# Kernel optimization log

Measured on AMD Instinct MI355X. Metric: run time of the kernel, lower is better.

Reference implementation:

```python
import jax, jax.numpy as jnp
import numpy as np

N_NODES = 100000
IMPROVED_FILL = 2.0  # PyG improved=True self-loop weight


def setup_inputs() -> dict:
    key = jax.random.key(0)
    k1, k2, k3, k4 = jax.random.split(key, 4)
    x = jax.random.normal(k1, (N_NODES, 128), dtype=jnp.float32)
    edge_index = jax.random.randint(k2, (2, 1600000), 0, N_NODES, dtype=jnp.int64)
    edge_weight = jax.random.uniform(k3, (1600000,), dtype=jnp.float32)
    W = jax.random.normal(k4, (128, 64), dtype=jnp.float32) * (1.0 / np.sqrt(128.0))
    b = jnp.zeros((64,), dtype=jnp.float32)
    return {"x": x, "edge_index": edge_index, "edge_weight": edge_weight, "W": W, "b": b}


def reference(x, edge_index, edge_weight, W, b):
    N = x.shape[0]
    row, col = edge_index[0], edge_index[1]
    # add self-loops with fill value 2.0 (improved=True)
    loop = jnp.arange(N, dtype=edge_index.dtype)
    row_f = jnp.concatenate([row, loop])
    col_f = jnp.concatenate([col, loop])
    ew_f = jnp.concatenate([edge_weight, jnp.full((N,), IMPROVED_FILL, dtype=x.dtype)])
    # symmetric degree normalization (degree computed at target/col, per PyG gcn_norm)
    deg = jax.ops.segment_sum(ew_f, col_f, num_segments=N)  # [N]
    dinv = jnp.where(deg > 0, jax.lax.rsqrt(deg), 0.0)
    norm = dinv[row_f] * ew_f * dinv[col_f]  # [E+N]
    # linear transform first, then gather-scale-scatter aggregation, then bias
    xw = x @ W  # [N, 64]
    msgs = xw[row_f] * norm[:, None]  # [E+N, 64]
    out = jax.ops.segment_sum(msgs, col_f, num_segments=N) + b  # [N, 64]
    # act is None -> returns (x, embedding), both equal to out
    return (out, out)
```

## Files before the change

kernel.cpp:

```cpp
#include <hip/hip_runtime.h>

#define F_IN 128
#define F_OUT 64

#define NBK_SHIFT 7
#define NB_MAX    800
#define CAP       2432
#define NBC_SHIFT 10
#define NBC_MAX   104
#define CAPC      17408
#define CHUNK     3200
#define CHB       6

__device__ __forceinline__ unsigned short f2bf(float f) {
    unsigned u = __float_as_uint(f);
    u += 0x7FFFu + ((u >> 16) & 1u);
    return (unsigned short)(u >> 16);
}
__device__ __forceinline__ float bf2f(unsigned short h) {
    return __uint_as_float((unsigned)h << 16);
}

typedef __attribute__((ext_vector_type(8))) short bf16x8;
typedef __attribute__((ext_vector_type(4))) float f32x4;

__global__ __launch_bounds__(256) void partA_kernel(const int* __restrict__ rowi,
                                                    const int* __restrict__ coli,
                                                    const float* __restrict__ ew,
                                                    int* __restrict__ gcurC,
                                                    unsigned long long* __restrict__ recM,
                                                    int E, int NBC) {
    __shared__ unsigned long long rec[CHUNK];
    __shared__ int off0[NBC_MAX];
    __shared__ int cur[NBC_MAX];
    __shared__ int gbase[NBC_MAX];
    __shared__ int ps[256];

    const int t = threadIdx.x;
    const int start = blockIdx.x * CHUNK;
    int cntE = E - start;
    if (cntE > CHUNK) cntE = CHUNK;
    if (cntE < 0) cntE = 0;

    for (int i = t; i < NBC; i += 256) cur[i] = 0;
    __syncthreads();

    #pragma unroll 4
    for (int i = t; i < cntE; i += 256)
        atomicAdd(&cur[coli[start + i] >> NBC_SHIFT], 1);
    __syncthreads();

    int v0 = 0, v1 = 0, v2 = 0, v3 = 0, tsum;
    {
        int b0 = t << 2;
        if (b0 + 0 < NBC) v0 = cur[b0 + 0];
        if (b0 + 1 < NBC) v1 = cur[b0 + 1];
        if (b0 + 2 < NBC) v2 = cur[b0 + 2];
        if (b0 + 3 < NBC) v3 = cur[b0 + 3];
    }
    tsum = v0 + v1 + v2 + v3;
    ps[t] = tsum;
    __syncthreads();
    for (int off = 1; off < 256; off <<= 1) {
        int a = (t >= off) ? ps[t - off] : 0;
        __syncthreads();
        ps[t] += a;
        __syncthreads();
    }
    {
        int e0 = ps[t] - tsum;
        int b0 = t << 2;
        if (b0 + 0 < NBC) off0[b0 + 0] = e0;           e0 += v0;
        if (b0 + 1 < NBC) off0[b0 + 1] = e0;           e0 += v1;
        if (b0 + 2 < NBC) off0[b0 + 2] = e0;           e0 += v2;
        if (b0 + 3 < NBC) off0[b0 + 3] = e0;
    }
    __syncthreads();

    for (int i = t; i < NBC; i += 256) {
        int c = cur[i];
        gbase[i] = (c > 0) ? atomicAdd(&gcurC[i], c) : 0;
        cur[i] = off0[i];
    }
    __syncthreads();

    #pragma unroll 2
    for (int i = t; i < cntE; i += 256) {
        int c = coli[start + i];
        int r = rowi[start + i];
        float w = ew[start + i];
        unsigned q = (unsigned)(w * 32767.0f + 0.5f);
        int b = c >> NBC_SHIFT;
        int p = atomicAdd(&cur[b], 1);
        rec[p] = ((unsigned long long)(unsigned)c << 32) |
                 (((unsigned)r << 15) | q);
    }
    __syncthreads();

    #pragma unroll 2
    for (int i = t; i < cntE; i += 256) {
        unsigned long long rv = rec[i];
        int c = (int)(rv >> 32);
        int b = c >> NBC_SHIFT;
        int gp = gbase[b] + (i - off0[b]);
        if (gp < CAPC) recM[(size_t)b * CAPC + gp] = rv;
    }
}

__global__ __launch_bounds__(1024) void deg_kernel(const int* __restrict__ gcurC,
                                                   const unsigned long long* __restrict__ recM,
                                                   float* __restrict__ degf, int N) {
    __shared__ int dsum[1024];
    const int t = threadIdx.x;
    const int cb = blockIdx.x;
    dsum[t] = 0;
    __syncthreads();

    int tot = gcurC[cb];
    if (tot > CAPC) tot = CAPC;
    const size_t mb = (size_t)cb * CAPC;

    #pragma unroll
    for (int j = 0; j < 17; ++j) {
        const int i = t + (j << 10);
        if (i < tot) {
            unsigned long long rv = recM[mb + i];
            int lc = (int)((unsigned)(rv >> 32) & 1023u);
            atomicAdd(&dsum[lc], (int)((unsigned)rv & 32767u));
        }
    }
    __syncthreads();

    const int c = (cb << NBC_SHIFT) + t;
    if (c < N) degf[c] = (float)dsum[t] * (1.f / 32767.f);
}

#define KP 136
#define OP 72

__global__ __launch_bounds__(256) void midfuse_kernel(const int* __restrict__ gcurC,
                                                      const unsigned long long* __restrict__ recM,
                                                      int* __restrict__ gcurF,
                                                      unsigned long long* __restrict__ recE,
                                                      const float* __restrict__ x,
                                                      const float* __restrict__ W,
                                                      const float* __restrict__ degf,
                                                      unsigned short* __restrict__ ybf,
                                                      int NPB, int N) {
    __shared__ unsigned long long sm[4352];
    const int t = threadIdx.x;

    if (blockIdx.x < NPB) {
        unsigned long long* rec = sm;
        int* cnt2 = (int*)(sm + CHUNK);
        int* inc2 = cnt2 + 128;
        int* cur2 = inc2 + 128;
        int* fstart = cur2 + 128;
        int* fbase = fstart + 8;

        const int cb = blockIdx.x / CHB;
        const int k  = blockIdx.x % CHB;

        int tot = gcurC[cb];
        if (tot > CAPC) tot = CAPC;
        const int s0 = k * CHUNK;
        int seg = tot - s0;
        if (seg > CHUNK) seg = CHUNK;
        if (seg <= 0) return;

        if (t < 128) cnt2[t] = 0;
        __syncthreads();

        const size_t mb = (size_t)cb * CAPC + s0;
        unsigned long long va[13];
        unsigned char vf[13];
        #pragma unroll
        for (int j = 0; j < 13; ++j) {
            const int i = t + (j << 8);
            if (i < seg) {
                unsigned long long rv = recM[mb + i];
                va[j] = rv;
                vf[j] = (unsigned char)(((unsigned)(rv >> 32) >> 7) & 7u);
                atomicAdd(&cnt2[((int)vf[j] << 4) | (t & 15)], 1);
            }
        }
        __syncthreads();

        if (t < 128) inc2[t] = cnt2[t];
        __syncthreads();
        for (int off = 1; off < 128; off <<= 1) {
            int vv = 0;
            if (t < 128 && t >= off) vv = inc2[t - off];
            __syncthreads();
            if (t < 128) inc2[t] += vv;
            __syncthreads();
        }
        if (t < 128) cur2[t] = inc2[t] - cnt2[t];
        __syncthreads();

        if (t < 8) {
            int st = (t == 0) ? 0 : inc2[((t - 1) << 4) | 15];
            int en = inc2[(t << 4) | 15];
            fstart[t] = st;
            int fc = en - st;
            fbase[t] = (fc > 0) ? atomicAdd(&gcurF[(cb << 3) + t], fc) : 0;
        }
        __syncthreads();

        #pragma unroll
        for (int j = 0; j < 13; ++j) {
            const int i = t + (j << 8);
            if (i < seg) {
                int p = atomicAdd(&cur2[((int)vf[j] << 4) | (t & 15)], 1);
                rec[p] = va[j];
            }
        }
        __syncthreads();

        for (int i = t; i < seg; i += 256) {
            unsigned long long rv = rec[i];
            int f = (int)(((unsigned)(rv >> 32) >> 7) & 7u);
            int gp = fbase[f] + (i - fstart[f]);
            if (gp < CAP) recE[(size_t)((cb << 3) + f) * CAP + gp] = rv;
        }
    } else {
        unsigned short* Wh = (unsigned short*)sm;
        unsigned short* Wl = Wh + 64 * KP;

        const int lane = t & 63;
        const int w    = t >> 6;
        const int base = (blockIdx.x - NPB) * 64;

        for (int i = t; i < F_IN * F_OUT; i += 256) {
            int k = i >> 6, c = i & 63;
            float f = W[i];
            unsigned short h = f2bf(f);
            Wh[c * KP + k] = h;
            Wl[c * KP + k] = f2bf(f - bf2f(h));
        }
        __syncthreads();

        const int rg = lane & 15;
        const int g  = lane >> 4;

        int row = base + 16 * w + rg;
        if (row > N - 1) row = N - 1;
        const float* xrow = x + (size_t)row * F_IN;

        f32x4 acc0 = {0.f, 0.f, 0.f, 0.f};
        f32x4 acc1 = acc0, acc2 = acc0, acc3 = acc0;

        #pragma unroll
        for (int ks = 0; ks < 4; ++ks) {
            const int k8 = ks * 32 + g * 8;
            float4 xa = *(const float4*)(xrow + k8);
            float4 xb = *(const float4*)(xrow + k8 + 4);
            float fs[8] = {xa.x, xa.y, xa.z, xa.w, xb.x, xb.y, xb.z, xb.w};
            bf16x8 ah, al;
            #pragma unroll
            for (int j = 0; j < 8; ++j) {
                unsigned short h = f2bf(fs[j]);
                ah[j] = (short)h;
                al[j] = (short)f2bf(fs[j] - bf2f(h));
            }
            #define DO_TILE(T, ACC) {                                          \
                const int cb_ = ((T) * 16 + rg) * KP + k8;                     \
                bf16x8 bh_ = *(const bf16x8*)&Wh[cb_];                         \
                bf16x8 bl_ = *(const bf16x8*)&Wl[cb_];                         \
                ACC = __builtin_amdgcn_mfma_f32_16x16x32_bf16(ah, bh_, ACC, 0,0,0);\
                ACC = __builtin_amdgcn_mfma_f32_16x16x32_bf16(al, bh_, ACC, 0,0,0);\
                ACC = __builtin_amdgcn_mfma_f32_16x16x32_bf16(ah, bl_, ACC, 0,0,0);\
            }
            DO_TILE(0, acc0) DO_TILE(1, acc1) DO_TILE(2, acc2) DO_TILE(3, acc3)
            #undef DO_TILE
        }

        float dv[4];
        #pragma unroll
        for (int i = 0; i < 4; ++i) {
            int rr = base + 16 * w + 4 * g + i;
            dv[i] = rsqrtf(2.0f + degf[(rr < N) ? rr : (N - 1)]);
        }

        __syncthreads();
        unsigned short* outl = (unsigned short*)sm;

        #define ST_TILE(T, ACC) {                                              \
            _Pragma("unroll")                                                  \
            for (int i = 0; i < 4; ++i)                                        \
                outl[(16 * w + 4 * g + i) * OP + (T) * 16 + rg] =              \
                    f2bf(ACC[i] * dv[i]);                                      \
        }
        ST_TILE(0, acc0) ST_TILE(1, acc1) ST_TILE(2, acc2) ST_TILE(3, acc3)
        #undef ST_TILE
        __syncthreads();

        #pragma unroll
        for (int rep = 0; rep < 2; ++rep) {
            int cid = t + (rep << 8);
            int r = cid >> 3, s = cid & 7;
            if (base + r < N) {
                uint4 val = *(const uint4*)&outl[r * OP + s * 8];
                *(uint4*)&ybf[((size_t)(base + r) << 6) + (s << 3)] = val;
            }
        }
    }
}

__global__ __launch_bounds__(512) void aggfuse_kernel(const int* __restrict__ gcur,
                                                      const unsigned long long* __restrict__ recE,
                                                      const unsigned short* __restrict__ ybf,
                                                      const float* __restrict__ degf,
                                                      const float* __restrict__ b,
                                                      float* __restrict__ out, int N) {
    __shared__ int cnt_s[128];
    __shared__ int inc_s[128];
    __shared__ int cur_s[128];
    __shared__ unsigned int lrec[CAP + 16];

    const int bq   = blockIdx.x >> 1;
    const int half = blockIdx.x & 1;
    const int t = threadIdx.x;
    if (t < 128) cnt_s[t] = 0;
    __syncthreads();

    int nE = gcur[bq];
    if (nE > CAP) nE = CAP;
    const size_t basee = (size_t)bq * CAP;

    unsigned va[5];
    unsigned char vc[5];
    #pragma unroll
    for (int j = 0; j < 5; ++j) {
        const int i = t + (j << 9);
        if (i < nE) {
            unsigned long long rv = recE[basee + i];
            va[j] = (unsigned)rv;
            vc[j] = (unsigned char)((unsigned)(rv >> 32) & 127u);
            atomicAdd(&cnt_s[vc[j]], 1);
        }
    }
    __syncthreads();

    if (t < 128) inc_s[t] = cnt_s[t];
    __syncthreads();
    for (int off = 1; off < 128; off <<= 1) {
        int vv = 0;
        if (t < 128 && t >= off) vv = inc_s[t - off];
        __syncthreads();
        if (t < 128) inc_s[t] += vv;
        __syncthreads();
    }
    if (t < 128) cur_s[t] = inc_s[t] - cnt_s[t];
    __syncthreads();

    #pragma unroll
    for (int j = 0; j < 5; ++j) {
        const int i = t + (j << 9);
        if (i < nE) {
            int p = atomicAdd(&cur_s[vc[j]], 1);
            lrec[p] = va[j];
        }
    }
    __syncthreads();

    const int lane = t & 63;
    const int w8   = t >> 6;
    const int es   = lane >> 4;
    const int fl   = lane & 15;
    const int c0   = bq << NBK_SHIFT;

    const float4 bb = *(const float4*)&b[fl << 2];

    for (int j = 0; j < 8; ++j) {
        const int lc = (half << 6) + w8 * 8 + j;
        const int v = c0 + lc;
        if (v >= N) break;

        const int n   = cnt_s[lc];
        const int off = inc_s[lc] - n;
        const float dv = rsqrtf(2.0f + degf[v]);
        const ushort4 yv = *(const ushort4*)&ybf[((size_t)v << 6) + (fl << 2)];

        float4 acc = {0, 0, 0, 0};
        const int nm1 = off + n - 1;
        for (int i = 0; i < n; i += 16) {
            const int q0 = off + i + es, q1 = q0 + 4, q2 = q0 + 8, q3 = q0 + 12;
            const bool k0 = q0 <= nm1, k1 = q1 <= nm1, k2 = q2 <= nm1, k3 = q3 <= nm1;
            unsigned m0 = lrec[k0 ? q0 : nm1];
            unsigned m1 = lrec[k1 ? q1 : nm1];
            unsigned m2 = lrec[k2 ? q2 : nm1];
            unsigned m3 = lrec[k3 ? q3 : nm1];
            ushort4 a0 = {0,0,0,0}, a1 = {0,0,0,0}, a2 = {0,0,0,0}, a3 = {0,0,0,0};
            if (k0) a0 = *(const ushort4*)&ybf[((size_t)(m0 >> 15) << 6) + (fl << 2)];
            if (k1) a1 = *(const ushort4*)&ybf[((size_t)(m1 >> 15) << 6) + (fl << 2)];
            if (k2) a2 = *(const ushort4*)&ybf[((size_t)(m2 >> 15) << 6) + (fl << 2)];
            if (k3) a3 = *(const ushort4*)&ybf[((size_t)(m3 >> 15) << 6) + (fl << 2)];
            if (k0) {
                float w0 = (float)(m0 & 32767u) * (1.f / 32767.f);
                acc.x = fmaf(w0, bf2f(a0.x), acc.x);
                acc.y = fmaf(w0, bf2f(a0.y), acc.y);
                acc.z = fmaf(w0, bf2f(a0.z), acc.z);
                acc.w = fmaf(w0, bf2f(a0.w), acc.w);
            }
            if (k1) {
                float w1 = (float)(m1 & 32767u) * (1.f / 32767.f);
                acc.x = fmaf(w1, bf2f(a1.x), acc.x);
                acc.y = fmaf(w1, bf2f(a1.y), acc.y);
                acc.z = fmaf(w1, bf2f(a1.z), acc.z);
                acc.w = fmaf(w1, bf2f(a1.w), acc.w);
            }
            if (k2) {
                float w2 = (float)(m2 & 32767u) * (1.f / 32767.f);
                acc.x = fmaf(w2, bf2f(a2.x), acc.x);
                acc.y = fmaf(w2, bf2f(a2.y), acc.y);
                acc.z = fmaf(w2, bf2f(a2.z), acc.z);
                acc.w = fmaf(w2, bf2f(a2.w), acc.w);
            }
            if (k3) {
                float w3 = (float)(m3 & 32767u) * (1.f / 32767.f);
                acc.x = fmaf(w3, bf2f(a3.x), acc.x);
                acc.y = fmaf(w3, bf2f(a3.y), acc.y);
                acc.z = fmaf(w3, bf2f(a3.z), acc.z);
                acc.w = fmaf(w3, bf2f(a3.w), acc.w);
            }
        }

        acc.x += __shfl_xor(acc.x, 16); acc.y += __shfl_xor(acc.y, 16);
        acc.z += __shfl_xor(acc.z, 16); acc.w += __shfl_xor(acc.w, 16);
        acc.x += __shfl_xor(acc.x, 32); acc.y += __shfl_xor(acc.y, 32);
        acc.z += __shfl_xor(acc.z, 32); acc.w += __shfl_xor(acc.w, 32);

        if (lane < 16) {
            float4 val;
            val.x = fmaf(dv, 2.f * bf2f(yv.x) + acc.x, bb.x);
            val.y = fmaf(dv, 2.f * bf2f(yv.y) + acc.y, bb.y);
            val.z = fmaf(dv, 2.f * bf2f(yv.z) + acc.z, bb.z);
            val.w = fmaf(dv, 2.f * bf2f(yv.w) + acc.w, bb.w);
            *(float4*)&out[((size_t)v << 6) + (fl << 2)]       = val;
            *(float4*)&out[((size_t)(N + v) << 6) + (fl << 2)] = val;
        }
    }
}

extern "C" void kernel_launch(void* const* d_in, const int* in_sizes, int n_in,
                              void* d_out, int out_size, void* d_ws, size_t ws_size,
                              hipStream_t stream) {
    const float* x  = (const float*)d_in[0];
    const int*   ei = (const int*)d_in[1];
    const float* ew = (const float*)d_in[2];
    const float* W  = (const float*)d_in[3];
    const float* b  = (const float*)d_in[4];

    const int N = in_sizes[0] / F_IN;
    const int E = in_sizes[2];

    const int* rowi = ei;
    const int* coli = ei + E;
    float* out = (float*)d_out;

    const int NBC = (N + 1023) >> NBC_SHIFT;
    const int NBF = (N + 127) >> NBK_SHIFT;
    if (NBF > NB_MAX || NBC > NBC_MAX) return;

    const int Npad = (N + 255) & ~255;
    char* p = (char*)d_ws;
    unsigned short* ybf = (unsigned short*)p;   p += (size_t)N * F_OUT * 2;
    unsigned long long* recM = (unsigned long long*)p; p += (size_t)NBC_MAX * CAPC * 8;
    unsigned long long* recE = (unsigned long long*)p; p += (size_t)NB_MAX * CAP * 8;
    int*   gcurC = (int*)p;                     p += (size_t)NBC_MAX * 4;
    int*   gcurF = (int*)p;                     p += (size_t)NB_MAX * 4;
    float* degf = (float*)p;                    p += (size_t)Npad * 4;

    hipMemsetAsync(gcurC, 0, ((size_t)NBC_MAX + NB_MAX) * sizeof(int), stream);

    const int P = (E + CHUNK - 1) / CHUNK;
    partA_kernel<<<P, 256, 0, stream>>>(rowi, coli, ew, gcurC, recM, E, NBC);
    deg_kernel<<<NBC, 1024, 0, stream>>>(gcurC, recM, degf, N);

    const int NPB = NBC * CHB;
    const int NGB = (N + 63) / 64;
    midfuse_kernel<<<NPB + NGB, 256, 0, stream>>>(gcurC, recM, gcurF, recE,
                                                  x, W, degf, ybf, NPB, N);

    aggfuse_kernel<<<NBF * 2, 512, 0, stream>>>(gcurF, recE, ybf, degf, b, out, N);
}
```

Baseline: 214.7 us.

## Overlap GEMM with edge bucketing and degree with fine partition, regroup kernels

The x@W GEMM blocks now run in the same launch as the coarse edge bucketing, so it no longer waits on the degree computation. The degree reduction shares a launch with the fine partition and stores dinv directly. Because the GEMM output is no longer pre-scaled by the source dinv, the aggregation kernel now gathers dinv per edge and multiplies it into the weight. Aggregation also uses half as many blocks, each handling 128 nodes instead of 64. This trades one fewer serial kernel stage for an extra random gather per edge and less parallelism in the aggregation step.

```diff
diff --git a/kernel.cpp b/kernel.cpp
--- a/kernel.cpp
+++ b/kernel.cpp
@@ -24,204 +24,95 @@
 typedef __attribute__((ext_vector_type(8))) short bf16x8;
 typedef __attribute__((ext_vector_type(4))) float f32x4;
 
-__global__ __launch_bounds__(256) void partA_kernel(const int* __restrict__ rowi,
+#define KP 136
+#define OP 72
+
+__global__ __launch_bounds__(256) void fuse1_kernel(const int* __restrict__ rowi,
                                                     const int* __restrict__ coli,
                                                     const float* __restrict__ ew,
                                                     int* __restrict__ gcurC,
                                                     unsigned long long* __restrict__ recM,
-                                                    int E, int NBC) {
-    __shared__ unsigned long long rec[CHUNK];
-    __shared__ int off0[NBC_MAX];
-    __shared__ int cur[NBC_MAX];
-    __shared__ int gbase[NBC_MAX];
-    __shared__ int ps[256];
-
-    const int t = threadIdx.x;
-    const int start = blockIdx.x * CHUNK;
-    int cntE = E - start;
-    if (cntE > CHUNK) cntE = CHUNK;
-    if (cntE < 0) cntE = 0;
-
-    for (int i = t; i < NBC; i += 256) cur[i] = 0;
-    __syncthreads();
-
-    #pragma unroll 4
-    for (int i = t; i < cntE; i += 256)
-        atomicAdd(&cur[coli[start + i] >> NBC_SHIFT], 1);
-    __syncthreads();
-
-    int v0 = 0, v1 = 0, v2 = 0, v3 = 0, tsum;
-    {
-        int b0 = t << 2;
-        if (b0 + 0 < NBC) v0 = cur[b0 + 0];
-        if (b0 + 1 < NBC) v1 = cur[b0 + 1];
-        if (b0 + 2 < NBC) v2 = cur[b0 + 2];
-        if (b0 + 3 < NBC) v3 = cur[b0 + 3];
-    }
-    tsum = v0 + v1 + v2 + v3;
-    ps[t] = tsum;
-    __syncthreads();
-    for (int off = 1; off < 256; off <<= 1) {
-        int a = (t >= off) ? ps[t - off] : 0;
-        __syncthreads();
-        ps[t] += a;
-        __syncthreads();
-    }
-    {
-        int e0 = ps[t] - tsum;
-        int b0 = t << 2;
-        if (b0 + 0 < NBC) off0[b0 + 0] = e0;           e0 += v0;
-        if (b0 + 1 < NBC) off0[b0 + 1] = e0;           e0 += v1;
-        if (b0 + 2 < NBC) off0[b0 + 2] = e0;           e0 += v2;
-        if (b0 + 3 < NBC) off0[b0 + 3] = e0;
-    }
-    __syncthreads();
-
-    for (int i = t; i < NBC; i += 256) {
-        int c = cur[i];
-        gbase[i] = (c > 0) ? atomicAdd(&gcurC[i], c) : 0;
-        cur[i] = off0[i];
-    }
-    __syncthreads();
-
-    #pragma unroll 2
-    for (int i = t; i < cntE; i += 256) {
-        int c = coli[start + i];
-        int r = rowi[start + i];
-        float w = ew[start + i];
-        unsigned q = (unsigned)(w * 32767.0f + 0.5f);
-        int b = c >> NBC_SHIFT;
-        int p = atomicAdd(&cur[b], 1);
-        rec[p] = ((unsigned long long)(unsigned)c << 32) |
-                 (((unsigned)r << 15) | q);
-    }
-    __syncthreads();
-
-    #pragma unroll 2
-    for (int i = t; i < cntE; i += 256) {
-        unsigned long long rv = rec[i];
-        int c = (int)(rv >> 32);
-        int b = c >> NBC_SHIFT;
-        int gp = gbase[b] + (i - off0[b]);
-        if (gp < CAPC) recM[(size_t)b * CAPC + gp] = rv;
-    }
-}
-
-__global__ __launch_bounds__(1024) void deg_kernel(const int* __restrict__ gcurC,
-                                                   const unsigned long long* __restrict__ recM,
-                                                   float* __restrict__ degf, int N) {
-    __shared__ int dsum[1024];
-    const int t = threadIdx.x;
-    const int cb = blockIdx.x;
-    dsum[t] = 0;
-    __syncthreads();
-
-    int tot = gcurC[cb];
-    if (tot > CAPC) tot = CAPC;
-    const size_t mb = (size_t)cb * CAPC;
-
-    #pragma unroll
-    for (int j = 0; j < 17; ++j) {
-        const int i = t + (j << 10);
-        if (i < tot) {
-            unsigned long long rv = recM[mb + i];
-            int lc = (int)((unsigned)(rv >> 32) & 1023u);
-            atomicAdd(&dsum[lc], (int)((unsigned)rv & 32767u));
-        }
-    }
-    __syncthreads();
-
-    const int c = (cb << NBC_SHIFT) + t;
-    if (c < N) degf[c] = (float)dsum[t] * (1.f / 32767.f);
-}
-
-#define KP 136
-#define OP 72
-
-__global__ __launch_bounds__(256) void midfuse_kernel(const int* __restrict__ gcurC,
-                                                      const unsigned long long* __restrict__ recM,
-                                                      int* __restrict__ gcurF,
-                                                      unsigned long long* __restrict__ recE,
-                                                      const float* __restrict__ x,
-                                                      const float* __restrict__ W,
-                                                      const float* __restrict__ degf,
-                                                      unsigned short* __restrict__ ybf,
-                                                      int NPB, int N) {
+                                                    const float* __restrict__ x,
+                                                    const float* __restrict__ W,
+                                                    unsigned short* __restrict__ ybf,
+                                                    int E, int NBC, int P, int N) {
     __shared__ unsigned long long sm[4352];
     const int t = threadIdx.x;
 
-    if (blockIdx.x < NPB) {
+    if (blockIdx.x < (unsigned)P) {
         unsigned long long* rec = sm;
-        int* cnt2 = (int*)(sm + CHUNK);
-        int* inc2 = cnt2 + 128;
-        int* cur2 = inc2 + 128;
-        int* fstart = cur2 + 128;
-        int* fbase = fstart + 8;
-
-        const int cb = blockIdx.x / CHB;
-        const int k  = blockIdx.x % CHB;
-
-        int tot = gcurC[cb];
-        if (tot > CAPC) tot = CAPC;
-        const int s0 = k * CHUNK;
-        int seg = tot - s0;
-        if (seg > CHUNK) seg = CHUNK;
-        if (seg <= 0) return;
-
-        if (t < 128) cnt2[t] = 0;
-        __syncthreads();
-
-        const size_t mb = (size_t)cb * CAPC + s0;
-        unsigned long long va[13];
-        unsigned char vf[13];
-        #pragma unroll
-        for (int j = 0; j < 13; ++j) {
-            const int i = t + (j << 8);
-            if (i < seg) {
-                unsigned long long rv = recM[mb + i];
-                va[j] = rv;
-                vf[j] = (unsigned char)(((unsigned)(rv >> 32) >> 7) & 7u);
-                atomicAdd(&cnt2[((int)vf[j] << 4) | (t & 15)], 1);
-            }
-        }
-        __syncthreads();
-
-        if (t < 128) inc2[t] = cnt2[t];
-        __syncthreads();
-        for (int off = 1; off < 128; off <<= 1) {
-            int vv = 0;
-            if (t < 128 && t >= off) vv = inc2[t - off];
+        int* off0  = (int*)(sm + CHUNK);
+        int* cur   = off0 + NBC_MAX;
+        int* gbase = cur + NBC_MAX;
+        int* ps    = gbase + NBC_MAX;
+
+        const int start = blockIdx.x * CHUNK;
+        int cntE = E - start;
+        if (cntE > CHUNK) cntE = CHUNK;
+        if (cntE < 0) cntE = 0;
+
+        for (int i = t; i < NBC; i += 256) cur[i] = 0;
+        __syncthreads();
+
+        #pragma unroll 4
+        for (int i = t; i < cntE; i += 256)
+            atomicAdd(&cur[coli[start + i] >> NBC_SHIFT], 1);
+        __syncthreads();
+
+        int v0 = 0, v1 = 0, v2 = 0, v3 = 0, tsum;
+        {
+            int b0 = t << 2;
+            if (b0 + 0 < NBC) v0 = cur[b0 + 0];
+            if (b0 + 1 < NBC) v1 = cur[b0 + 1];
+            if (b0 + 2 < NBC) v2 = cur[b0 + 2];
+            if (b0 + 3 < NBC) v3 = cur[b0 + 3];
+        }
+        tsum = v0 + v1 + v2 + v3;
+        ps[t] = tsum;
+        __syncthreads();
+        for (int off = 1; off < 256; off <<= 1) {
+            int a = (t >= off) ? ps[t - off] : 0;
             __syncthreads();
-            if (t < 128) inc2[t] += vv;
+            ps[t] += a;
             __syncthreads();
         }
-        if (t < 128) cur2[t] = inc2[t] - cnt2[t];
-        __syncthreads();
-
-        if (t < 8) {
-            int st = (t == 0) ? 0 : inc2[((t - 1) << 4) | 15];
-            int en = inc2[(t << 4) | 15];
-            fstart[t] = st;
-            int fc = en - st;
-            fbase[t] = (fc > 0) ? atomicAdd(&gcurF[(cb << 3) + t], fc) : 0;
-        }
-        __syncthreads();
-
-        #pragma unroll
-        for (int j = 0; j < 13; ++j) {
-            const int i = t + (j << 8);
-            if (i < seg) {
-                int p = atomicAdd(&cur2[((int)vf[j] << 4) | (t & 15)], 1);
-                rec[p] = va[j];
-            }
-        }
-        __syncthreads();
-
-        for (int i = t; i < seg; i += 256) {
+        {
+            int e0 = ps[t] - tsum;
+            int b0 = t << 2;
+            if (b0 + 0 < NBC) off0[b0 + 0] = e0;       e0 += v0;
+            if (b0 + 1 < NBC) off0[b0 + 1] = e0;       e0 += v1;
+            if (b0 + 2 < NBC) off0[b0 + 2] = e0;       e0 += v2;
+            if (b0 + 3 < NBC) off0[b0 + 3] = e0;
+        }
+        __syncthreads();
+
+        for (int i = t; i < NBC; i += 256) {
+            int c = cur[i];
+            gbase[i] = (c > 0) ? atomicAdd(&gcurC[i], c) : 0;
+            cur[i] = off0[i];
+        }
+        __syncthreads();
+
+        #pragma unroll 2
+        for (int i = t; i < cntE; i += 256) {
+            int c = coli[start + i];
+            int r = rowi[start + i];
+            float w = ew[start + i];
+            unsigned q = (unsigned)(w * 32767.0f + 0.5f);
+            int b = c >> NBC_SHIFT;
+            int p = atomicAdd(&cur[b], 1);
+            rec[p] = ((unsigned long long)(unsigned)c << 32) |
+                     (((unsigned)r << 15) | q);
+        }
+        __syncthreads();
+
+        #pragma unroll 2
+        for (int i = t; i < cntE; i += 256) {
             unsigned long long rv = rec[i];
-            int f = (int)(((unsigned)(rv >> 32) >> 7) & 7u);
-            int gp = fbase[f] + (i - fstart[f]);
-            if (gp < CAP) recE[(size_t)((cb << 3) + f) * CAP + gp] = rv;
+            int c = (int)(rv >> 32);
+            int b = c >> NBC_SHIFT;
+            int gp = gbase[b] + (i - off0[b]);
+            if (gp < CAPC) recM[(size_t)b * CAPC + gp] = rv;
         }
     } else {
         unsigned short* Wh = (unsigned short*)sm;
@@ -229,7 +120,7 @@
 
         const int lane = t & 63;
         const int w    = t >> 6;
-        const int base = (blockIdx.x - NPB) * 64;
+        const int base = (blockIdx.x - P) * 64;
 
         for (int i = t; i < F_IN * F_OUT; i += 256) {
             int k = i >> 6, c = i & 63;
@@ -275,13 +166,6 @@
             #undef DO_TILE
         }
 
-        float dv[4];
-        #pragma unroll
-        for (int i = 0; i < 4; ++i) {
-            int rr = base + 16 * w + 4 * g + i;
-            dv[i] = rsqrtf(2.0f + degf[(rr < N) ? rr : (N - 1)]);
-        }
-
         __syncthreads();
         unsigned short* outl = (unsigned short*)sm;
 
@@ -289,7 +173,7 @@
             _Pragma("unroll")                                                  \
             for (int i = 0; i < 4; ++i)                                        \
                 outl[(16 * w + 4 * g + i) * OP + (T) * 16 + rg] =              \
-                    f2bf(ACC[i] * dv[i]);                                      \
+                    f2bf(ACC[i]);                                              \
         }
         ST_TILE(0, acc0) ST_TILE(1, acc1) ST_TILE(2, acc2) ST_TILE(3, acc3)
         #undef ST_TILE
@@ -307,10 +191,120 @@
     }
 }
 
+__global__ __launch_bounds__(256) void fuse2_kernel(const int* __restrict__ gcurC,
+                                                    const unsigned long long* __restrict__ recM,
+                                                    int* __restrict__ gcurF,
+                                                    unsigned long long* __restrict__ recE,
+                                                    float* __restrict__ dinvf,
+                                                    int NBC, int N) {
+    __shared__ unsigned long long sm[4352];
+    const int t = threadIdx.x;
+
+    if (blockIdx.x < (unsigned)NBC) {
+        int* dsum = (int*)sm;
+        const int cb = blockIdx.x;
+        for (int i = t; i < 1024; i += 256) dsum[i] = 0;
+        __syncthreads();
+
+        int tot = gcurC[cb];
+        if (tot > CAPC) tot = CAPC;
+        const size_t mb = (size_t)cb * CAPC;
+
+        for (int i = t; i < tot; i += 256) {
+            unsigned long long rv = recM[mb + i];
+            int lc = (int)((unsigned)(rv >> 32) & 1023u);
+            atomicAdd(&dsum[lc], (int)((unsigned)rv & 32767u));
+        }
+        __syncthreads();
+
+        for (int i = t; i < 1024; i += 256) {
+            const int c = (cb << NBC_SHIFT) + i;
+            if (c < N) {
+                float sw = (float)dsum[i] * (1.f / 32767.f);
+                dinvf[c] = rsqrtf(2.0f + sw);
+            }
+        }
+    } else {
+        unsigned long long* rec = sm;
+        int* cnt2 = (int*)(sm + CHUNK);
+        int* inc2 = cnt2 + 128;
+        int* cur2 = inc2 + 128;
+        int* fstart = cur2 + 128;
+        int* fbase = fstart + 8;
+
+        const int bid = blockIdx.x - NBC;
+        const int cb = bid / CHB;
+        const int k  = bid % CHB;
+
+        int tot = gcurC[cb];
+        if (tot > CAPC) tot = CAPC;
+        const int s0 = k * CHUNK;
+        int seg = tot - s0;
+        if (seg > CHUNK) seg = CHUNK;
+        if (seg <= 0) return;
+
+        if (t < 128) cnt2[t] = 0;
+        __syncthreads();
+
+        const size_t mb = (size_t)cb * CAPC + s0;
+        unsigned long long va[13];
+        unsigned char vf[13];
+        #pragma unroll
+        for (int j = 0; j < 13; ++j) {
+            const int i = t + (j << 8);
+            if (i < seg) {
+                unsigned long long rv = recM[mb + i];
+                va[j] = rv;
+                vf[j] = (unsigned char)(((unsigned)(rv >> 32) >> 7) & 7u);
+                atomicAdd(&cnt2[((int)vf[j] << 4) | (t & 15)], 1);
+            }
+        }
+        __syncthreads();
+
+        if (t < 128) inc2[t] = cnt2[t];
+        __syncthreads();
+        for (int off = 1; off < 128; off <<= 1) {
+            int vv = 0;
+            if (t < 128 && t >= off) vv = inc2[t - off];
+            __syncthreads();
+            if (t < 128) inc2[t] += vv;
+            __syncthreads();
+        }
+        if (t < 128) cur2[t] = inc2[t] - cnt2[t];
+        __syncthreads();
+
+        if (t < 8) {
+            int st = (t == 0) ? 0 : inc2[((t - 1) << 4) | 15];
+            int en = inc2[(t << 4) | 15];
+            fstart[t] = st;
+            int fc = en - st;
+            fbase[t] = (fc > 0) ? atomicAdd(&gcurF[(cb << 3) + t], fc) : 0;
+        }
+        __syncthreads();
+
+        #pragma unroll
+        for (int j = 0; j < 13; ++j) {
+            const int i = t + (j << 8);
+            if (i < seg) {
+                int p = atomicAdd(&cur2[((int)vf[j] << 4) | (t & 15)], 1);
+                rec[p] = va[j];
+            }
+        }
+        __syncthreads();
+
+        for (int i = t; i < seg; i += 256) {
+            unsigned long long rv = rec[i];
+            int f = (int)(((unsigned)(rv >> 32) >> 7) & 7u);
+            int gp = fbase[f] + (i - fstart[f]);
+            if (gp < CAP) recE[(size_t)((cb << 3) + f) * CAP + gp] = rv;
+        }
+    }
+}
+
 __global__ __launch_bounds__(512) void aggfuse_kernel(const int* __restrict__ gcur,
                                                       const unsigned long long* __restrict__ recE,
                                                       const unsigned short* __restrict__ ybf,
-                                                      const float* __restrict__ degf,
+                                                      const float* __restrict__ dinvf,
                                                       const float* __restrict__ b,
                                                       float* __restrict__ out, int N) {
     __shared__ int cnt_s[128];
@@ -318,8 +312,7 @@
     __shared__ int cur_s[128];
     __shared__ unsigned int lrec[CAP + 16];
 
-    const int bq   = blockIdx.x >> 1;
-    const int half = blockIdx.x & 1;
+    const int bq = blockIdx.x;
     const int t = threadIdx.x;
     if (t < 128) cnt_s[t] = 0;
     __syncthreads();
@@ -372,14 +365,14 @@
 
     const float4 bb = *(const float4*)&b[fl << 2];
 
-    for (int j = 0; j < 8; ++j) {
-        const int lc = (half << 6) + w8 * 8 + j;
+    for (int j = 0; j < 16; ++j) {
+        const int lc = w8 * 16 + j;
         const int v = c0 + lc;
         if (v >= N) break;
 
         const int n   = cnt_s[lc];
         const int off = inc_s[lc] - n;
-        const float dv = rsqrtf(2.0f + degf[v]);
+        const float dv = dinvf[v];
         const ushort4 yv = *(const ushort4*)&ybf[((size_t)v << 6) + (fl << 2)];
 
         float4 acc = {0, 0, 0, 0};
@@ -391,34 +384,38 @@
             unsigned m1 = lrec[k1 ? q1 : nm1];
             unsigned m2 = lrec[k2 ? q2 : nm1];
             unsigned m3 = lrec[k3 ? q3 : nm1];
+            float d0 = k0 ? dinvf[m0 >> 15] : 0.f;
+            float d1 = k1 ? dinvf[m1 >> 15] : 0.f;
+            float d2 = k2 ? dinvf[m2 >> 15] : 0.f;
+            float d3 = k3 ? dinvf[m3 >> 15] : 0.f;
             ushort4 a0 = {0,0,0,0}, a1 = {0,0,0,0}, a2 = {0,0,0,0}, a3 = {0,0,0,0};
             if (k0) a0 = *(const ushort4*)&ybf[((size_t)(m0 >> 15) << 6) + (fl << 2)];
             if (k1) a1 = *(const ushort4*)&ybf[((size_t)(m1 >> 15) << 6) + (fl << 2)];
             if (k2) a2 = *(const ushort4*)&ybf[((size_t)(m2 >> 15) << 6) + (fl << 2)];
             if (k3) a3 = *(const ushort4*)&ybf[((size_t)(m3 >> 15) << 6) + (fl << 2)];
             if (k0) {
-                float w0 = (float)(m0 & 32767u) * (1.f / 32767.f);
+                float w0 = (float)(m0 & 32767u) * (1.f / 32767.f) * d0;
                 acc.x = fmaf(w0, bf2f(a0.x), acc.x);
                 acc.y = fmaf(w0, bf2f(a0.y), acc.y);
                 acc.z = fmaf(w0, bf2f(a0.z), acc.z);
                 acc.w = fmaf(w0, bf2f(a0.w), acc.w);
             }
             if (k1) {
-                float w1 = (float)(m1 & 32767u) * (1.f / 32767.f);
+                float w1 = (float)(m1 & 32767u) * (1.f / 32767.f) * d1;
                 acc.x = fmaf(w1, bf2f(a1.x), acc.x);
                 acc.y = fmaf(w1, bf2f(a1.y), acc.y);
                 acc.z = fmaf(w1, bf2f(a1.z), acc.z);
                 acc.w = fmaf(w1, bf2f(a1.w), acc.w);
             }
             if (k2) {
-                float w2 = (float)(m2 & 32767u) * (1.f / 32767.f);
+                float w2 = (float)(m2 & 32767u) * (1.f / 32767.f) * d2;
                 acc.x = fmaf(w2, bf2f(a2.x), acc.x);
                 acc.y = fmaf(w2, bf2f(a2.y), acc.y);
                 acc.z = fmaf(w2, bf2f(a2.z), acc.z);
                 acc.w = fmaf(w2, bf2f(a2.w), acc.w);
             }
             if (k3) {
-                float w3 = (float)(m3 & 32767u) * (1.f / 32767.f);
+                float w3 = (float)(m3 & 32767u) * (1.f / 32767.f) * d3;
                 acc.x = fmaf(w3, bf2f(a3.x), acc.x);
                 acc.y = fmaf(w3, bf2f(a3.y), acc.y);
                 acc.z = fmaf(w3, bf2f(a3.z), acc.z);
@@ -432,11 +429,12 @@
         acc.z += __shfl_xor(acc.z, 32); acc.w += __shfl_xor(acc.w, 32);
 
         if (lane < 16) {
+            const float s2 = 2.f * dv * dv;
             float4 val;
-            val.x = fmaf(dv, 2.f * bf2f(yv.x) + acc.x, bb.x);
-            val.y = fmaf(dv, 2.f * bf2f(yv.y) + acc.y, bb.y);
-            val.z = fmaf(dv, 2.f * bf2f(yv.z) + acc.z, bb.z);
-            val.w = fmaf(dv, 2.f * bf2f(yv.w) + acc.w, bb.w);
+            val.x = fmaf(s2, bf2f(yv.x), fmaf(dv, acc.x, bb.x));
+            val.y = fmaf(s2, bf2f(yv.y), fmaf(dv, acc.y, bb.y));
+            val.z = fmaf(s2, bf2f(yv.z), fmaf(dv, acc.z, bb.z));
+            val.w = fmaf(s2, bf2f(yv.w), fmaf(dv, acc.w, bb.w));
             *(float4*)&out[((size_t)v << 6) + (fl << 2)]       = val;
             *(float4*)&out[((size_t)(N + v) << 6) + (fl << 2)] = val;
         }
@@ -470,18 +468,18 @@
     unsigned long long* recE = (unsigned long long*)p; p += (size_t)NB_MAX * CAP * 8;
     int*   gcurC = (int*)p;                     p += (size_t)NBC_MAX * 4;
     int*   gcurF = (int*)p;                     p += (size_t)NB_MAX * 4;
-    float* degf = (float*)p;                    p += (size_t)Npad * 4;
+    float* dinvf = (float*)p;                   p += (size_t)Npad * 4;
 
     hipMemsetAsync(gcurC, 0, ((size_t)NBC_MAX + NB_MAX) * sizeof(int), stream);
 
-    const int P = (E + CHUNK - 1) / CHUNK;
-    partA_kernel<<<P, 256, 0, stream>>>(rowi, coli, ew, gcurC, recM, E, NBC);
-    deg_kernel<<<NBC, 1024, 0, stream>>>(gcurC, recM, degf, N);
+    const int P   = (E + CHUNK - 1) / CHUNK;
+    const int NGB = (N + 63) / 64;
+    fuse1_kernel<<<P + NGB, 256, 0, stream>>>(rowi, coli, ew, gcurC, recM,
+                                              x, W, ybf, E, NBC, P, N);
 
     const int NPB = NBC * CHB;
-    const int NGB = (N + 63) / 64;
-    midfuse_kernel<<<NPB + NGB, 256, 0, stream>>>(gcurC, recM, gcurF, recE,
-                                                  x, W, degf, ybf, NPB, N);
-
-    aggfuse_kernel<<<NBF * 2, 512, 0, stream>>>(gcurF, recE, ybf, degf, b, out, N);
-}
+    fuse2_kernel<<<NBC + NPB, 256, 0, stream>>>(gcurC, recM, gcurF, recE,
+                                                dinvf, NBC, N);
+
+    aggfuse_kernel<<<NBF, 512, 0, stream>>>(gcurF, recE, ybf, dinvf, b, out, N);
+}
```

New measurement: 216.4 us. Within noise of the previous version (+0.8%).
